# Kernel tuning notes

Hardware: AMD Instinct MI355X
Metric: run time of the kernel (lower is better)

The kernel has to match this reference:

```python
import jax, jax.numpy as jnp
import numpy as np

B, S, G, E = 2048, 32768, 4096, 1024  # batch, source_size, n_groups(target_size), embeddings_size


def setup_inputs() -> dict:
    key = jax.random.key(0)
    k_x, k_w, k_we, k_perm = jax.random.split(key, 4)
    x = jax.random.normal(k_x, (B, S), dtype=jnp.float32)
    W = jax.random.normal(k_w, (E, G), dtype=jnp.float32) * 0.02  # Linear(target_size -> embed, no bias)
    # per-element weights for 'w_sum' groups (concatenated Linear(group_size,1) weights)
    w_elem = jax.random.normal(k_we, (S,), dtype=jnp.float32) * 0.1
    perm = jax.random.permutation(k_perm, S).astype(jnp.int32)
    # ragged group boundaries: n_groups groups, each size >= 1, summing to S
    rng = np.random.default_rng(0)
    cuts = np.sort(rng.choice(np.arange(1, S), G - 1, replace=False))
    sizes = np.diff(np.concatenate([[0], cuts, [S]]))
    segment_ids = jnp.asarray(np.repeat(np.arange(G), sizes), dtype=jnp.int32)
    # aggregation type per group: 0='sum', 1='or', 2='w_sum'
    agg_type = jnp.asarray(rng.integers(0, 3, G), dtype=jnp.int32)
    return {"x": x, "W": W, "w_elem": w_elem, "perm": perm,
            "segment_ids": segment_ids, "agg_type": agg_type}


def reference(x, W, w_elem, perm, segment_ids, agg_type):
    # gather via groups_permute
    xp = x[:, perm]  # [B, S]
    # fused ragged per-group reductions, segment axis first: [S, B] -> [G, B]
    xt = xp.T
    seg_sum = jax.ops.segment_sum(xt, segment_ids, num_segments=G)              # jnp.sum per group
    seg_wsum = jax.ops.segment_sum(xt * w_elem[:, None], segment_ids, num_segments=G)  # Linear(g,1) per group
    seg_nnz = jax.ops.segment_sum((xt != 0).astype(x.dtype), segment_ids, num_segments=G)
    seg_or = (seg_nnz > 0).astype(x.dtype)                                       # jnp.any per group (bool -> float on hstack)
    a = agg_type[:, None]
    y = jnp.where(a == 0, seg_sum, jnp.where(a == 1, seg_or, seg_wsum)).T        # [B, G]
    # relu + Linear(target_size -> embeddings_size, no bias)
    return jnp.einsum('bg,eg->be', jax.nn.relu(y), W)
```

## Files before the change

kernel.cpp:

```cpp
#include <hip/hip_runtime.h>
#include <hip/hip_bf16.h>

#define B_DIM 2048
#define S_DIM 32768
#define G_DIM 4096
#define E_DIM 1024
#define KSPLIT 4
#define KCHUNK (G_DIM / KSPLIT)

typedef __bf16 bf16x8 __attribute__((ext_vector_type(8)));
typedef float f32x4 __attribute__((ext_vector_type(4)));

__device__ __forceinline__ unsigned short f2bf(float f) {
  unsigned int u = __builtin_bit_cast(unsigned int, f);
  u += 0x7FFFu + ((u >> 16) & 1u);
  return (unsigned short)(u >> 16);
}

__device__ __forceinline__ float bfl(unsigned u) {
  return __builtin_bit_cast(float, u << 16);
}
__device__ __forceinline__ float bfh(unsigned u) {
  return __builtin_bit_cast(float, u & 0xFFFF0000u);
}

__device__ __forceinline__ void async16(void* lds, const void* g) {
  __builtin_amdgcn_global_load_lds(
      (const __attribute__((address_space(1))) unsigned int*)g,
      (__attribute__((address_space(3))) unsigned int*)lds, 16, 0, 0);
}

__device__ __forceinline__ void lds_add(float* p, float v) {
  unsigned off = (unsigned)(size_t)(__attribute__((address_space(3))) float*)p;
  asm volatile("ds_add_f32 %0, %1" :: "v"(off), "v"(v));
}

__global__ __launch_bounds__(256) void setup_meta(
    const float* __restrict__ w_elem, const int* __restrict__ perm,
    const int* __restrict__ segid, const int* __restrict__ agg,
    unsigned* __restrict__ meta1) {
  int s = blockIdx.x * 256 + threadIdx.x;
  if (s >= S_DIM) return;
  int g = segid[s];
  int a = agg[g];
  float cm = (a == 0) ? 1.0f : (a == 2 ? w_elem[s] : 0.0f);
  meta1[s] = (unsigned)perm[s] | (a == 1 ? 0x8000u : 0u) |
             ((unsigned)f2bf(cm) << 16);
}

__global__ __launch_bounds__(256) void setup_runs(
    const int* __restrict__ segid, unsigned* __restrict__ metaH,
    unsigned short* __restrict__ metaG) {
  int t = blockIdx.x * 256 + threadIdx.x;
  if (t >= S_DIM / 32) return;
  int s0 = t * 32;
  int prev = (s0 == 0) ? -1 : segid[s0 - 1];
  unsigned m = 0;
#pragma unroll
  for (int c = 0; c < 8; ++c) {
    int4 gw = *reinterpret_cast<const int4*>(segid + s0 + c * 4);
    if (gw.x != prev) m |= 1u << (c * 4 + 0);
    if (gw.y != gw.x) m |= 1u << (c * 4 + 1);
    if (gw.z != gw.y) m |= 1u << (c * 4 + 2);
    if (gw.w != gw.z) m |= 1u << (c * 4 + 3);
    prev = gw.w;
  }
  metaH[t] = m;
  metaG[t] = (unsigned short)segid[s0];
}

__global__ __launch_bounds__(256) void conv_w(const float* __restrict__ W,
                                              unsigned short* __restrict__ Wb) {
  size_t i = ((size_t)blockIdx.x * 256 + threadIdx.x) * 4;
  float4 v = *reinterpret_cast<const float4*>(W + i);
  ushort4 o;
  o.x = f2bf(v.x);
  o.y = f2bf(v.y);
  o.z = f2bf(v.z);
  o.w = f2bf(v.w);
  *reinterpret_cast<ushort4*>(Wb + i) = o;
}

__global__ __launch_bounds__(1024, 8) void seg_reduce(
    const float* __restrict__ x, const unsigned* __restrict__ meta1,
    const unsigned* __restrict__ metaH, const unsigned short* __restrict__ metaG,
    const int* __restrict__ agg, unsigned short* __restrict__ y) {
  __shared__ __align__(16) unsigned short xrow[S_DIM];
  __shared__ float acc[G_DIM];
  const int t = threadIdx.x;
  const int b = blockIdx.x;
  const unsigned lane = t & 63;

#pragma unroll
  for (int i = 0; i < G_DIM / 1024; ++i) acc[t + i * 1024] = 0.0f;

  const unsigned mrun = metaH[t];
  const bool fp = (mrun & 1u) != 0;
  const int g0 = metaG[t];
  int g = g0;

  const float4* xg = reinterpret_cast<const float4*>(x + (size_t)b * S_DIM);
#pragma unroll
  for (int i = 0; i < S_DIM / 4 / 1024; ++i) {
    float4 v = xg[i * 1024 + t];
    unsigned short h0 = __builtin_bit_cast(unsigned short, (__bf16)v.x);
    unsigned short h1 = __builtin_bit_cast(unsigned short, (__bf16)v.y);
    unsigned short h2 = __builtin_bit_cast(unsigned short, (__bf16)v.z);
    unsigned short h3 = __builtin_bit_cast(unsigned short, (__bf16)v.w);
    uint2 p;
    p.x = (unsigned)h0 | ((unsigned)h1 << 16);
    p.y = (unsigned)h2 | ((unsigned)h3 << 16);
    *reinterpret_cast<uint2*>(&xrow[(i * 1024 + t) * 4]) = p;
  }
  __syncthreads();

  const int s0 = t * 32;
  float sum = 0.0f, lead = 0.0f;
  int nf = 0;

  for (int h = 0; h < 2; ++h) {
    const int sb = s0 + h * 16;
    uint4 ma = *reinterpret_cast<const uint4*>(meta1 + sb);
    uint4 mb = *reinterpret_cast<const uint4*>(meta1 + sb + 4);
    uint4 mc = *reinterpret_cast<const uint4*>(meta1 + sb + 8);
    uint4 md = *reinterpret_cast<const uint4*>(meta1 + sb + 12);
    unsigned m[16] = {ma.x, ma.y, ma.z, ma.w, mb.x, mb.y, mb.z, mb.w,
                      mc.x, mc.y, mc.z, mc.w, md.x, md.y, md.z, md.w};
    unsigned short xu[16];
#pragma unroll
    for (int j = 0; j < 16; ++j) xu[j] = xrow[m[j] & 0x7FFF];
    const unsigned mh = mrun >> (h * 16);
#pragma unroll
    for (int j = 0; j < 16; ++j) {
      if (h + j > 0 && (mh & (1u << j))) {
        if (nf == 0 && !fp) {
          lead = sum;
        } else {
          acc[g] = sum;
        }
        ++nf;
        sum = 0.0f;
        ++g;
      }
      float xv = bfl((unsigned)xu[j]);
      float cm = bfh(m[j]);
      float v = (m[j] & 0x8000u) ? (xu[j] ? 1.0f : 0.0f) : xv * cm;
      sum += v;
    }
  }
  float myLead = fp ? 0.0f : (nf == 0 ? sum : lead);
  const int F = (mrun != 0);

  float s = myLead;
  int o = !F;
#pragma unroll
  for (int d = 1; d <= 32; d <<= 1) {
    float sd = __shfl_down(s, d);
    int od = __shfl_down(o, d);
    const bool valid = lane + d < 64;
    sd = valid ? sd : 0.0f;
    od = valid ? od : 1;
    s += o ? sd : 0.0f;
    o &= od;
  }
  float s1 = __shfl_down(s, 1);
  int o1 = __shfl_down(o, 1);
  if (lane == 63) {
    s1 = 0.0f;
    o1 = 1;
  }

  if (mrun != 0) {
    float tot = sum + s1;
    if (o1) {
      lds_add(&acc[g], tot);
    } else {
      acc[g] = tot;
    }
  }
  if (lane == 0 && !fp) {
    lds_add(&acc[g0], s);
  }

  asm volatile("s_waitcnt lgkmcnt(0)" ::: "memory");
  __syncthreads();

#pragma unroll
  for (int i = 0; i < G_DIM / 1024; ++i) {
    int g2 = t + i * 1024;
    float v = acc[g2];
    if (agg[g2] == 1) v = (v > 0.0f) ? 1.0f : 0.0f;
    v = fmaxf(v, 0.0f);
    y[(size_t)b * G_DIM + g2] = f2bf(v);
  }
}

__global__ __launch_bounds__(256) void gemm_bt(
    const unsigned short* __restrict__ A,
    const unsigned short* __restrict__ Bw,
    unsigned short* __restrict__ part) {
  __shared__ __align__(16) unsigned short As[64 * 64];
  __shared__ __align__(16) unsigned short Bs[64 * 64];
  const int t = threadIdx.x;
  const int lane = t & 63;
  const int wid = t >> 6;
  const int wr = wid >> 1;
  const int wc = wid & 1;
  const int row0 = blockIdx.y * 64;
  const int col0 = blockIdx.x * 64;
  const int kc = blockIdx.z;

  const int r_ = t >> 3;
  const int s_ = t & 7;
  const int ksw = (s_ ^ (r_ & 7)) * 8;
  const unsigned short* Ag0 = A + (size_t)(row0 + r_) * G_DIM + ksw;
  const unsigned short* Ag1 = A + (size_t)(row0 + r_ + 32) * G_DIM + ksw;
  const unsigned short* Bg0 = Bw + (size_t)(col0 + r_) * G_DIM + ksw;
  const unsigned short* Bg1 = Bw + (size_t)(col0 + r_ + 32) * G_DIM + ksw;

  char* AsB = (char*)As;
  char* BsB = (char*)Bs;
  char* dA0 = AsB + wid * 1024;
  char* dA1 = AsB + 4096 + wid * 1024;
  char* dB0 = BsB + wid * 1024;
  char* dB1 = BsB + 4096 + wid * 1024;

  const int lm = lane & 15;
  const int lk = lane >> 4;

  f32x4 acc[2][2] = {};

  for (int kt = kc * KCHUNK; kt < (kc + 1) * KCHUNK; kt += 64) {
    async16(dA0, Ag0 + kt);
    async16(dA1, Ag1 + kt);
    async16(dB0, Bg0 + kt);
    async16(dB1, Bg1 + kt);
    __syncthreads();
#pragma unroll
    for (int kk = 0; kk < 2; ++kk) {
      bf16x8 af[2], bfr[2];
#pragma unroll
      for (int m = 0; m < 2; ++m) {
        int row = wr * 32 + m * 16 + lm;
        int slot = (kk * 4 + lk) ^ (row & 7);
        af[m] = *(const bf16x8*)(AsB + row * 128 + slot * 16);
      }
#pragma unroll
      for (int n = 0; n < 2; ++n) {
        int row = wc * 32 + n * 16 + lm;
        int slot = (kk * 4 + lk) ^ (row & 7);
        bfr[n] = *(const bf16x8*)(BsB + row * 128 + slot * 16);
      }
#pragma unroll
      for (int m = 0; m < 2; ++m)
#pragma unroll
        for (int n = 0; n < 2; ++n)
          acc[m][n] = __builtin_amdgcn_mfma_f32_16x16x32_bf16(af[m], bfr[n],
                                                              acc[m][n], 0, 0, 0);
    }
    __syncthreads();
  }

  unsigned short* P = part + (size_t)kc * B_DIM * E_DIM;
#pragma unroll
  for (int m = 0; m < 2; ++m) {
    int r = row0 + wr * 32 + m * 16 + lk * 4;
#pragma unroll
    for (int n = 0; n < 2; ++n) {
      int c = col0 + wc * 32 + n * 16 + lm;
#pragma unroll
      for (int q = 0; q < 4; ++q) {
        P[(size_t)(r + q) * E_DIM + c] = f2bf(acc[m][n][q]);
      }
    }
  }
}

__global__ __launch_bounds__(256) void reduce_part(
    const unsigned short* __restrict__ part, float* __restrict__ C) {
  const size_t i = ((size_t)blockIdx.x * 256 + threadIdx.x) * 8;
  const size_t n = (size_t)B_DIM * E_DIM;
  float e[8] = {};
#pragma unroll
  for (int p = 0; p < KSPLIT; ++p) {
    uint4 v = *reinterpret_cast<const uint4*>(part + p * n + i);
    unsigned w[4] = {v.x, v.y, v.z, v.w};
#pragma unroll
    for (int q = 0; q < 4; ++q) {
      e[2 * q] += bfl(w[q]);
      e[2 * q + 1] += bfh(w[q]);
    }
  }
  float4 o0 = {e[0], e[1], e[2], e[3]};
  float4 o1 = {e[4], e[5], e[6], e[7]};
  *reinterpret_cast<float4*>(C + i) = o0;
  *reinterpret_cast<float4*>(C + i + 4) = o1;
}

extern "C" void kernel_launch(void* const* d_in, const int* in_sizes, int n_in,
                              void* d_out, int out_size, void* d_ws, size_t ws_size,
                              hipStream_t stream) {
  const float* x = (const float*)d_in[0];
  const float* W = (const float*)d_in[1];
  const float* w_elem = (const float*)d_in[2];
  const int* perm = (const int*)d_in[3];
  const int* segid = (const int*)d_in[4];
  const int* agg = (const int*)d_in[5];
  float* out = (float*)d_out;

  char* ws = (char*)d_ws;
  unsigned short* y = (unsigned short*)ws;
  unsigned short* Wb =
      (unsigned short*)(ws + (size_t)B_DIM * G_DIM * 2);
  unsigned short* part =
      (unsigned short*)(ws + (size_t)B_DIM * G_DIM * 2 +
                        (size_t)E_DIM * G_DIM * 2);
  unsigned* meta1 =
      (unsigned*)((char*)part + (size_t)KSPLIT * B_DIM * E_DIM * 2);
  unsigned* metaH = (unsigned*)((char*)meta1 + (size_t)S_DIM * 4);
  unsigned short* metaG = (unsigned short*)((char*)metaH + (S_DIM / 32) * 4);

  hipLaunchKernelGGL(setup_meta, dim3(S_DIM / 256), dim3(256), 0, stream,
                     w_elem, perm, segid, agg, meta1);
  hipLaunchKernelGGL(setup_runs, dim3((S_DIM / 32) / 256), dim3(256), 0,
                     stream, segid, metaH, metaG);
  hipLaunchKernelGGL(conv_w, dim3((E_DIM * G_DIM / 4) / 256), dim3(256), 0,
                     stream, W, Wb);
  hipLaunchKernelGGL(seg_reduce, dim3(B_DIM), dim3(1024), 0, stream, x, meta1,
                     metaH, metaG, agg, y);
  hipLaunchKernelGGL(gemm_bt, dim3(E_DIM / 64, B_DIM / 64, KSPLIT), dim3(256),
                     0, stream, y, Wb, part);
  hipLaunchKernelGGL(reduce_part,
                     dim3(((size_t)B_DIM * E_DIM / 8) / 256), dim3(256), 0,
                     stream, part, out);
}
```

Before: 125.4 us.

## Warp-specialize seg_reduce with producer/consumer double-buffered rows

```diff
diff --git a/kernel.cpp b/kernel.cpp
--- a/kernel.cpp
+++ b/kernel.cpp
@@ -7,6 +7,7 @@
 #define E_DIM 1024
 #define KSPLIT 4
 #define KCHUNK (G_DIM / KSPLIT)
+#define ROWS 8
 
 typedef __bf16 bf16x8 __attribute__((ext_vector_type(8)));
 typedef float f32x4 __attribute__((ext_vector_type(4)));
@@ -33,6 +34,15 @@
 __device__ __forceinline__ void lds_add(float* p, float v) {
   unsigned off = (unsigned)(size_t)(__attribute__((address_space(3))) float*)p;
   asm volatile("ds_add_f32 %0, %1" :: "v"(off), "v"(v));
+}
+
+__device__ __forceinline__ uint2 pack4bf(float4 v) {
+  uint2 r;
+  r.x = (unsigned)__builtin_bit_cast(unsigned short, (__bf16)v.x) |
+        ((unsigned)__builtin_bit_cast(unsigned short, (__bf16)v.y) << 16);
+  r.y = (unsigned)__builtin_bit_cast(unsigned short, (__bf16)v.z) |
+        ((unsigned)__builtin_bit_cast(unsigned short, (__bf16)v.w) << 16);
+  return r;
 }
 
 __global__ __launch_bounds__(256) void setup_meta(
@@ -81,117 +91,159 @@
   *reinterpret_cast<ushort4*>(Wb + i) = o;
 }
 
-__global__ __launch_bounds__(1024, 8) void seg_reduce(
+__global__ __launch_bounds__(1024, 4) void seg_reduce(
     const float* __restrict__ x, const unsigned* __restrict__ meta1,
     const unsigned* __restrict__ metaH, const unsigned short* __restrict__ metaG,
     const int* __restrict__ agg, unsigned short* __restrict__ y) {
-  __shared__ __align__(16) unsigned short xrow[S_DIM];
-  __shared__ float acc[G_DIM];
+  __shared__ __align__(16) unsigned short xbuf[2][S_DIM];
+  __shared__ float acc[2][G_DIM];
   const int t = threadIdx.x;
-  const int b = blockIdx.x;
+  const int wid = t >> 6;
   const unsigned lane = t & 63;
-
-#pragma unroll
-  for (int i = 0; i < G_DIM / 1024; ++i) acc[t + i * 1024] = 0.0f;
-
-  const unsigned mrun = metaH[t];
-  const bool fp = (mrun & 1u) != 0;
-  const int g0 = metaG[t];
-  int g = g0;
-
-  const float4* xg = reinterpret_cast<const float4*>(x + (size_t)b * S_DIM);
-#pragma unroll
-  for (int i = 0; i < S_DIM / 4 / 1024; ++i) {
-    float4 v = xg[i * 1024 + t];
-    unsigned short h0 = __builtin_bit_cast(unsigned short, (__bf16)v.x);
-    unsigned short h1 = __builtin_bit_cast(unsigned short, (__bf16)v.y);
-    unsigned short h2 = __builtin_bit_cast(unsigned short, (__bf16)v.z);
-    unsigned short h3 = __builtin_bit_cast(unsigned short, (__bf16)v.w);
-    uint2 p;
-    p.x = (unsigned)h0 | ((unsigned)h1 << 16);
-    p.y = (unsigned)h2 | ((unsigned)h3 << 16);
-    *reinterpret_cast<uint2*>(&xrow[(i * 1024 + t) * 4]) = p;
-  }
+  const int b0 = blockIdx.x * ROWS;
+  const bool producer = (wid < 8);
+  const int ci = t - 512;
+
+  unsigned mr0 = 0, mr1 = 0;
+  int g0 = 0;
+  int ar[8];
+  if (!producer) {
+    uint2 hh = *reinterpret_cast<const uint2*>(metaH + ci * 2);
+    mr0 = hh.x;
+    mr1 = hh.y;
+    g0 = metaG[ci * 2];
+#pragma unroll
+    for (int i = 0; i < 8; ++i) ar[i] = agg[ci + i * 512];
+#pragma unroll
+    for (int i = 0; i < 8; ++i) {
+      acc[0][ci + i * 512] = 0.0f;
+      acc[1][ci + i * 512] = 0.0f;
+    }
+  } else {
+    const float4* xg = reinterpret_cast<const float4*>(x + (size_t)b0 * S_DIM);
+    const int base = wid * 1024;
+#pragma unroll
+    for (int k = 0; k < 16; ++k) {
+      float4 v = xg[base + k * 64 + lane];
+      uint2 p = pack4bf(v);
+      *reinterpret_cast<uint2*>(&xbuf[0][(base + k * 64 + lane) * 4]) = p;
+    }
+  }
+  const unsigned long long mrun = (unsigned long long)mr0 |
+                                  ((unsigned long long)mr1 << 32);
+  const bool fp = (mrun & 1ULL) != 0;
+  const int F = (mrun != 0ULL);
   __syncthreads();
 
-  const int s0 = t * 32;
-  float sum = 0.0f, lead = 0.0f;
-  int nf = 0;
-
-  for (int h = 0; h < 2; ++h) {
-    const int sb = s0 + h * 16;
-    uint4 ma = *reinterpret_cast<const uint4*>(meta1 + sb);
-    uint4 mb = *reinterpret_cast<const uint4*>(meta1 + sb + 4);
-    uint4 mc = *reinterpret_cast<const uint4*>(meta1 + sb + 8);
-    uint4 md = *reinterpret_cast<const uint4*>(meta1 + sb + 12);
-    unsigned m[16] = {ma.x, ma.y, ma.z, ma.w, mb.x, mb.y, mb.z, mb.w,
-                      mc.x, mc.y, mc.z, mc.w, md.x, md.y, md.z, md.w};
-    unsigned short xu[16];
-#pragma unroll
-    for (int j = 0; j < 16; ++j) xu[j] = xrow[m[j] & 0x7FFF];
-    const unsigned mh = mrun >> (h * 16);
-#pragma unroll
-    for (int j = 0; j < 16; ++j) {
-      if (h + j > 0 && (mh & (1u << j))) {
-        if (nf == 0 && !fp) {
-          lead = sum;
+  for (int r = 0; r < ROWS; ++r) {
+    if (producer) {
+      if (r + 1 < ROWS) {
+        const float4* xg =
+            reinterpret_cast<const float4*>(x + (size_t)(b0 + r + 1) * S_DIM);
+        unsigned short* xb = xbuf[(r + 1) & 1];
+        const int base = wid * 1024;
+#pragma unroll
+        for (int k = 0; k < 16; ++k) {
+          float4 v = xg[base + k * 64 + lane];
+          uint2 p = pack4bf(v);
+          *reinterpret_cast<uint2*>(&xb[(base + k * 64 + lane) * 4]) = p;
+        }
+      }
+    } else {
+      if (r > 0) {
+        float* ap = acc[(r - 1) & 1];
+        const size_t yb = (size_t)(b0 + r - 1) * G_DIM;
+#pragma unroll
+        for (int i = 0; i < 8; ++i) {
+          int g2 = ci + i * 512;
+          float v = ap[g2];
+          if (ar[i] == 1) v = (v > 0.0f) ? 1.0f : 0.0f;
+          y[yb + g2] = f2bf(fmaxf(v, 0.0f));
+          ap[g2] = 0.0f;
+        }
+      }
+      const unsigned short* xr = xbuf[r & 1];
+      float* ac = acc[r & 1];
+      const int s0 = ci * 64;
+      int g = g0;
+      float sum = 0.0f, lead = 0.0f;
+      int nf = 0;
+#pragma unroll
+      for (int c = 0; c < 4; ++c) {
+        const int sb = s0 + c * 16;
+        uint4 ma = *reinterpret_cast<const uint4*>(meta1 + sb);
+        uint4 mb = *reinterpret_cast<const uint4*>(meta1 + sb + 4);
+        uint4 mc = *reinterpret_cast<const uint4*>(meta1 + sb + 8);
+        uint4 md = *reinterpret_cast<const uint4*>(meta1 + sb + 12);
+        unsigned m[16] = {ma.x, ma.y, ma.z, ma.w, mb.x, mb.y, mb.z, mb.w,
+                          mc.x, mc.y, mc.z, mc.w, md.x, md.y, md.z, md.w};
+        unsigned short xu[16];
+#pragma unroll
+        for (int j = 0; j < 16; ++j) xu[j] = xr[m[j] & 0x7FFF];
+#pragma unroll
+        for (int j = 0; j < 16; ++j) {
+          const int e = c * 16 + j;
+          if (e > 0 && ((mrun >> e) & 1ULL)) {
+            if (nf == 0 && !fp) {
+              lead = sum;
+            } else {
+              ac[g] = sum;
+            }
+            ++nf;
+            sum = 0.0f;
+            ++g;
+          }
+          float xv = bfl((unsigned)xu[j]);
+          float cm = bfh(m[j]);
+          float v = (m[j] & 0x8000u) ? (xu[j] ? 1.0f : 0.0f) : xv * cm;
+          sum += v;
+        }
+      }
+      float myLead = fp ? 0.0f : (nf == 0 ? sum : lead);
+      float s = myLead;
+      int o = !F;
+#pragma unroll
+      for (int d = 1; d <= 32; d <<= 1) {
+        float sd = __shfl_down(s, d);
+        int od = __shfl_down(o, d);
+        const bool valid = lane + d < 64;
+        sd = valid ? sd : 0.0f;
+        od = valid ? od : 1;
+        s += o ? sd : 0.0f;
+        o &= od;
+      }
+      float s1 = __shfl_down(s, 1);
+      int o1 = __shfl_down(o, 1);
+      if (lane == 63) {
+        s1 = 0.0f;
+        o1 = 1;
+      }
+      if (F) {
+        float tot = sum + s1;
+        if (o1) {
+          lds_add(&ac[g], tot);
         } else {
-          acc[g] = sum;
+          ac[g] = tot;
         }
-        ++nf;
-        sum = 0.0f;
-        ++g;
-      }
-      float xv = bfl((unsigned)xu[j]);
-      float cm = bfh(m[j]);
-      float v = (m[j] & 0x8000u) ? (xu[j] ? 1.0f : 0.0f) : xv * cm;
-      sum += v;
-    }
-  }
-  float myLead = fp ? 0.0f : (nf == 0 ? sum : lead);
-  const int F = (mrun != 0);
-
-  float s = myLead;
-  int o = !F;
-#pragma unroll
-  for (int d = 1; d <= 32; d <<= 1) {
-    float sd = __shfl_down(s, d);
-    int od = __shfl_down(o, d);
-    const bool valid = lane + d < 64;
-    sd = valid ? sd : 0.0f;
-    od = valid ? od : 1;
-    s += o ? sd : 0.0f;
-    o &= od;
-  }
-  float s1 = __shfl_down(s, 1);
-  int o1 = __shfl_down(o, 1);
-  if (lane == 63) {
-    s1 = 0.0f;
-    o1 = 1;
-  }
-
-  if (mrun != 0) {
-    float tot = sum + s1;
-    if (o1) {
-      lds_add(&acc[g], tot);
-    } else {
-      acc[g] = tot;
-    }
-  }
-  if (lane == 0 && !fp) {
-    lds_add(&acc[g0], s);
-  }
-
-  asm volatile("s_waitcnt lgkmcnt(0)" ::: "memory");
-  __syncthreads();
-
-#pragma unroll
-  for (int i = 0; i < G_DIM / 1024; ++i) {
-    int g2 = t + i * 1024;
-    float v = acc[g2];
-    if (agg[g2] == 1) v = (v > 0.0f) ? 1.0f : 0.0f;
-    v = fmaxf(v, 0.0f);
-    y[(size_t)b * G_DIM + g2] = f2bf(v);
+      }
+      if (lane == 0 && !fp) {
+        lds_add(&ac[g0], s);
+      }
+      asm volatile("s_waitcnt lgkmcnt(0)" ::: "memory");
+    }
+    __syncthreads();
+  }
+
+  if (!producer) {
+    float* ap = acc[(ROWS - 1) & 1];
+    const size_t yb = (size_t)(b0 + ROWS - 1) * G_DIM;
+#pragma unroll
+    for (int i = 0; i < 8; ++i) {
+      int g2 = ci + i * 512;
+      float v = ap[g2];
+      if (ar[i] == 1) v = (v > 0.0f) ? 1.0f : 0.0f;
+      y[yb + g2] = f2bf(fmaxf(v, 0.0f));
+    }
   }
 }
 
@@ -326,8 +378,8 @@
                      stream, segid, metaH, metaG);
   hipLaunchKernelGGL(conv_w, dim3((E_DIM * G_DIM / 4) / 256), dim3(256), 0,
                      stream, W, Wb);
-  hipLaunchKernelGGL(seg_reduce, dim3(B_DIM), dim3(1024), 0, stream, x, meta1,
-                     metaH, metaG, agg, y);
+  hipLaunchKernelGGL(seg_reduce, dim3(B_DIM / ROWS), dim3(1024), 0, stream, x,
+                     meta1, metaH, metaG, agg, y);
   hipLaunchKernelGGL(gemm_bt, dim3(E_DIM / 64, B_DIM / 64, KSPLIT), dim3(256),
                      0, stream, y, Wb, part);
   hipLaunchKernelGGL(reduce_part,
```

Result: slower. 139.4 us (+11.2%).
